# Kernel tuning notes

Measured on AMD Instinct MI355X. Metric: run time of the kernel, lower is better.

Reference implementation:

```python
import jax, jax.numpy as jnp
import numpy as np

HEADS = 4
DIM_HEAD = 64


def _rope(x, inv_freq):
    """Interleaved rotary embedding over axis -2 (time). x: (N, h, T, d)."""
    T = x.shape[-2]
    t = jnp.arange(T, dtype=x.dtype)
    f = t[:, None] * inv_freq[None, :].astype(x.dtype)   # (T, d/2)
    f = jnp.repeat(f, 2, axis=-1)                        # (T, d), interleaved pairs
    cos, sin = jnp.cos(f), jnp.sin(f)
    x1, x2 = x[..., 0::2], x[..., 1::2]
    rot = jnp.stack([-x2, x1], axis=-1).reshape(x.shape)  # rotate_half, interleaved
    return x * cos + rot * sin


def setup_inputs() -> dict:
    key = jax.random.key(0)
    k1, k2, k3, k4 = jax.random.split(key, 4)
    B, T, H, W, D = 2, 64, 32, 32, 256
    inner = HEADS * DIM_HEAD
    x = jax.random.normal(k1, (B, T, H, W, D), dtype=jnp.float32)
    w_qkv = jax.random.normal(k2, (D, 3 * inner), dtype=jnp.float32) * 0.02
    w_out = jax.random.normal(k3, (inner, D), dtype=jnp.float32) * 0.02
    b_out = jax.random.normal(k4, (D,), dtype=jnp.float32) * 0.02
    # rotary-embedding-torch default: 1 / theta^(arange(0, d, 2)/d)
    inv_freq = (1.0 / (10000.0 ** (np.arange(0, DIM_HEAD, 2) / DIM_HEAD))).astype(np.float32)
    return {"x": x, "w_qkv": w_qkv, "w_out": w_out, "b_out": b_out,
            "inv_freq": jnp.asarray(inv_freq)}


def reference(x, w_qkv, w_out, b_out, inv_freq):
    B, T, H, W, D = x.shape
    h, d = HEADS, DIM_HEAD
    qkv = x @ w_qkv                                   # (B,T,H,W,3*inner)
    q, k, v = jnp.split(qkv, 3, axis=-1)

    def to_heads(t_):
        # B T H W (h d) -> (B H W) h T d
        t_ = t_.reshape(B, T, H, W, h, d)
        return t_.transpose(0, 2, 3, 4, 1, 5).reshape(B * H * W, h, T, d)

    q, k, v = map(to_heads, (q, k, v))
    q = _rope(q, inv_freq)
    k = _rope(k, inv_freq)

    scale = 1.0 / np.sqrt(d).astype(np.float32)
    scores = jnp.einsum('nhtd,nhsd->nhts', q, k) * scale  # (BHW, h, T, T)
    causal = jnp.tril(jnp.ones((T, T), dtype=bool))
    scores = jnp.where(causal, scores, jnp.finfo(scores.dtype).min)
    attn = jax.nn.softmax(scores, axis=-1)
    o = jnp.einsum('nhts,nhsd->nhtd', attn, v)            # (BHW, h, T, d)

    # (B H W) h T d -> B T H W (h d)
    o = o.reshape(B, H, W, h, T, d).transpose(0, 4, 1, 2, 3, 5).reshape(B, T, H, W, h * d)
    return o @ w_out + b_out
```

## Files before the change

kernel.cpp:

```cpp
#include <hip/hip_runtime.h>
#include <hip/hip_bf16.h>

typedef __bf16 bf16_t;
typedef bf16_t bf16x4 __attribute__((ext_vector_type(4)));
typedef bf16_t bf16x8 __attribute__((ext_vector_type(8)));
typedef float f32x4 __attribute__((ext_vector_type(4)));
typedef unsigned int u32;

#define MFMA16(a, b, c) __builtin_amdgcn_mfma_f32_16x16x32_bf16((a), (b), (c), 0, 0, 0)

__device__ __forceinline__ int sxi(int row, int e) { return row * 256 + (e ^ ((row & 7) << 3)); }
__device__ __forceinline__ int ski(int row, int e) { return row * 64 + (e ^ ((row & 7) << 3)); }

__device__ __forceinline__ u32 pk2(float a, float b) {
  union { bf16_t h[2]; u32 u; } x;
  x.h[0] = (bf16_t)a; x.h[1] = (bf16_t)b;
  return x.u;
}

__global__ void transpose_to_bf16(const float* __restrict__ in, bf16_t* __restrict__ outp,
                                  int K, int N) {
  __shared__ float tile[32][33];
  const int k0 = blockIdx.x * 32;
  const int n0 = blockIdx.y * 32;
  const int tx = threadIdx.x;
  const int ty = threadIdx.y;
#pragma unroll
  for (int i = 0; i < 32; i += 8)
    tile[ty + i][tx] = in[(size_t)(k0 + ty + i) * N + (n0 + tx)];
  __syncthreads();
#pragma unroll
  for (int i = 0; i < 32; i += 8)
    outp[(size_t)(n0 + ty + i) * K + (k0 + tx)] = (bf16_t)tile[tx][ty + i];
}

__global__ void rope_table(const float* __restrict__ invf, float2* __restrict__ cs) {
  const int idx = blockIdx.x * 256 + threadIdx.x;
  const int t = idx >> 5;
  const int i = idx & 31;
  const float f = (float)t * invf[i];
  cs[idx] = make_float2(cosf(f), sinf(f));
}

__global__ __launch_bounds__(256) void taa_fused(
    const float* __restrict__ x, const bf16_t* __restrict__ wqkvT,
    const bf16_t* __restrict__ woutT, const float* __restrict__ bout,
    const float2* __restrict__ ropecs, float* __restrict__ out) {
  __shared__ __attribute__((aligned(16))) bf16_t sX[64 * 256];

  const int tid = threadIdx.x;
  const int w = tid >> 6;
  const int l = tid & 63;
  const int l16 = l & 15;
  const int g = l >> 4;

  const int site = blockIdx.x;
  const int b = site >> 10;
  const int sp = site & 1023;

  const size_t TS = 1024 * 256;
  const float* xp = x + (size_t)((b * 64) * 1024 + sp) * 256;
  float* op = out + (size_t)((b * 64) * 1024 + sp) * 256;

#pragma unroll
  for (int it = 0; it < 16; ++it) {
    const int idx = tid + it * 256;
    const int t = idx >> 6;
    const int c = (idx & 63) * 4;
    const float4 v = *(const float4*)(xp + (size_t)t * TS + c);
    bf16x4 o4;
    o4[0] = (bf16_t)v.x; o4[1] = (bf16_t)v.y; o4[2] = (bf16_t)v.z; o4[3] = (bf16_t)v.w;
    *(bf16x4*)&sX[sxi(t, c)] = o4;
  }
  __syncthreads();

  u32 qtb[4][4][2];
  {
    f32x4 qt[4][4] = {};
#pragma unroll
    for (int k0 = 0; k0 < 256; k0 += 32) {
      const int ko = k0 + 8 * g;
      bf16x8 aw[4], bx[4];
#pragma unroll
      for (int m = 0; m < 4; ++m)
        aw[m] = *(const bf16x8*)&wqkvT[(size_t)(w * 64 + 16 * m + l16) * 256 + ko];
#pragma unroll
      for (int n = 0; n < 4; ++n) bx[n] = *(const bf16x8*)&sX[sxi(16 * n + l16, ko)];
#pragma unroll
      for (int m = 0; m < 4; ++m)
#pragma unroll
        for (int n = 0; n < 4; ++n) qt[m][n] = MFMA16(aw[m], bx[n], qt[m][n]);
    }
    const float qs = 0.125f * 1.44269504088896f;
#pragma unroll
    for (int m = 0; m < 4; ++m)
#pragma unroll
      for (int n = 0; n < 4; ++n)
#pragma unroll
        for (int c = 0; c < 2; ++c) {
          const float v0 = qt[m][n][2 * c], v1 = qt[m][n][2 * c + 1];
          const float2 cs = ropecs[(16 * n + l16) * 32 + 8 * m + 2 * g + c];
          qtb[m][n][c] = pk2((v0 * cs.x - v1 * cs.y) * qs, (v1 * cs.x + v0 * cs.y) * qs);
        }
  }

  u32 kb[4][4][2];
  {
    f32x4 ka[4][4] = {};
#pragma unroll
    for (int k0 = 0; k0 < 256; k0 += 32) {
      const int ko = k0 + 8 * g;
      bf16x8 ax[4];
#pragma unroll
      for (int m = 0; m < 4; ++m) ax[m] = *(const bf16x8*)&sX[sxi(16 * m + l16, ko)];
#pragma unroll
      for (int n = 0; n < 4; ++n) {
        const bf16x8 bw = *(const bf16x8*)&wqkvT[(size_t)(256 + w * 64 + 16 * n + l16) * 256 + ko];
#pragma unroll
        for (int m = 0; m < 4; ++m) ka[m][n] = MFMA16(ax[m], bw, ka[m][n]);
      }
    }
#pragma unroll
    for (int m = 0; m < 4; ++m)
#pragma unroll
      for (int n = 0; n < 4; ++n) {
        f32x4 kr;
#pragma unroll
        for (int r = 0; r < 4; ++r) {
          const float v = ka[m][n][r];
          const float p = __shfl_xor(v, 1);
          const int s = 16 * m + 4 * g + r;
          const int dd = 16 * n + l16;
          const float2 cs = ropecs[s * 32 + 8 * n + (l16 >> 1)];
          kr[r] = (dd & 1) ? (v * cs.x + p * cs.y) : (v * cs.x - p * cs.y);
        }
#pragma unroll
        for (int c = 0; c < 2; ++c) kb[m][n][c] = pk2(kr[2 * c], kr[2 * c + 1]);
      }
  }

  u32 vb[4][4][2];
  {
    f32x4 va[4][4] = {};
#pragma unroll
    for (int k0 = 0; k0 < 256; k0 += 32) {
      const int ko = k0 + 8 * g;
      bf16x8 ax[4];
#pragma unroll
      for (int m = 0; m < 4; ++m) ax[m] = *(const bf16x8*)&sX[sxi(16 * m + l16, ko)];
#pragma unroll
      for (int n = 0; n < 4; ++n) {
        const bf16x8 bw = *(const bf16x8*)&wqkvT[(size_t)(512 + w * 64 + 16 * n + l16) * 256 + ko];
#pragma unroll
        for (int m = 0; m < 4; ++m) va[m][n] = MFMA16(ax[m], bw, va[m][n]);
      }
    }
#pragma unroll
    for (int m = 0; m < 4; ++m)
#pragma unroll
      for (int n = 0; n < 4; ++n)
#pragma unroll
        for (int c = 0; c < 2; ++c) vb[m][n][c] = pk2(va[m][n][2 * c], va[m][n][2 * c + 1]);
  }
  __syncthreads();

  bf16_t* slice = &sX[w * 4096];
#pragma unroll
  for (int m = 0; m < 4; ++m)
#pragma unroll
    for (int n = 0; n < 4; ++n)
#pragma unroll
      for (int c = 0; c < 2; ++c) {
        union { u32 u; bf16_t h[2]; } uz;
        uz.u = kb[m][n][c];
        slice[ski(16 * m + 4 * g + 2 * c, 16 * n + l16)] = uz.h[0];
        slice[ski(16 * m + 4 * g + 2 * c + 1, 16 * n + l16)] = uz.h[1];
      }

  f32x4 sc[4][4] = {};
#pragma unroll
  for (int ks = 0; ks < 2; ++ks) {
    const int ko = ks * 32 + 8 * g;
    bf16x8 ak[4];
#pragma unroll
    for (int m = 0; m < 4; ++m) ak[m] = *(const bf16x8*)&slice[ski(16 * m + l16, ko)];
#pragma unroll
    for (int n = 0; n < 4; ++n) {
      union { u32 u[4]; bf16x8 v; } uu;
#pragma unroll
      for (int k2 = 0; k2 < 4; ++k2) {
        const int src = ((((2 * g + (k2 >> 1)) & 3) << 4) | l16);
        const u32 a0 = (u32)__shfl((int)qtb[2 * ks][n][k2 & 1], src);
        const u32 a1 = (u32)__shfl((int)qtb[2 * ks + 1][n][k2 & 1], src);
        uu.u[k2] = (g & 2) ? a1 : a0;
      }
#pragma unroll
      for (int m = 0; m < 4; ++m) sc[m][n] = MFMA16(ak[m], uu.v, sc[m][n]);
    }
  }

#pragma unroll
  for (int n = 0; n < 4; ++n) {
    const int t = 16 * n + l16;
    float vals[16];
    float mx = -3.0e38f;
#pragma unroll
    for (int m = 0; m < 4; ++m)
#pragma unroll
      for (int r = 0; r < 4; ++r) {
        const int s = 16 * m + 4 * g + r;
        const float v = (s <= t) ? sc[m][n][r] : -3.0e38f;
        vals[4 * m + r] = v;
        mx = fmaxf(mx, v);
      }
    mx = fmaxf(mx, __shfl_xor(mx, 16));
    mx = fmaxf(mx, __shfl_xor(mx, 32));
    float sum = 0.f;
#pragma unroll
    for (int i = 0; i < 16; ++i) {
      vals[i] = exp2f(vals[i] - mx);
      sum += vals[i];
    }
    sum += __shfl_xor(sum, 16);
    sum += __shfl_xor(sum, 32);
    const float inv = 1.0f / sum;
#pragma unroll
    for (int m = 0; m < 4; ++m) {
      bf16x4 p4;
#pragma unroll
      for (int r = 0; r < 4; ++r) p4[r] = (bf16_t)(vals[4 * m + r] * inv);
      *(bf16x4*)&slice[ski(t, 16 * m + 4 * g)] = p4;
    }
  }

  f32x4 oacc[4][4] = {};
#pragma unroll
  for (int ks = 0; ks < 2; ++ks) {
    const int ko = ks * 32 + 8 * g;
    bf16x8 ap[4];
#pragma unroll
    for (int m = 0; m < 4; ++m) ap[m] = *(const bf16x8*)&slice[ski(16 * m + l16, ko)];
#pragma unroll
    for (int n = 0; n < 4; ++n) {
      union { u32 u[4]; bf16x8 v; } uu;
#pragma unroll
      for (int k2 = 0; k2 < 4; ++k2) {
        const int src = ((((2 * g + (k2 >> 1)) & 3) << 4) | l16);
        const u32 a0 = (u32)__shfl((int)vb[2 * ks][n][k2 & 1], src);
        const u32 a1 = (u32)__shfl((int)vb[2 * ks + 1][n][k2 & 1], src);
        uu.u[k2] = (g & 2) ? a1 : a0;
      }
#pragma unroll
      for (int m = 0; m < 4; ++m) oacc[m][n] = MFMA16(ap[m], uu.v, oacc[m][n]);
    }
  }
  __syncthreads();

#pragma unroll
  for (int m = 0; m < 4; ++m)
#pragma unroll
    for (int n = 0; n < 4; ++n)
#pragma unroll
      for (int r = 0; r < 4; ++r)
        sX[sxi(16 * m + 4 * g + r, w * 64 + 16 * n + l16)] = (bf16_t)oacc[m][n][r];
  __syncthreads();

  f32x4 acc[4][4] = {};
#pragma unroll
  for (int k0 = 0; k0 < 256; k0 += 32) {
    const int ko = k0 + 8 * g;
    bf16x8 af[4];
#pragma unroll
    for (int m = 0; m < 4; ++m) af[m] = *(const bf16x8*)&sX[sxi(16 * m + l16, ko)];
#pragma unroll
    for (int n = 0; n < 4; ++n) {
      const bf16x8 bw = *(const bf16x8*)&woutT[(size_t)(w * 64 + 16 * n + l16) * 256 + ko];
#pragma unroll
      for (int m = 0; m < 4; ++m) acc[m][n] = MFMA16(af[m], bw, acc[m][n]);
    }
  }
  float bb[4];
#pragma unroll
  for (int n = 0; n < 4; ++n) bb[n] = bout[w * 64 + 16 * n + l16];
#pragma unroll
  for (int m = 0; m < 4; ++m)
#pragma unroll
    for (int n = 0; n < 4; ++n)
#pragma unroll
      for (int r = 0; r < 4; ++r) {
        const int t = 16 * m + 4 * g + r;
        const int col = w * 64 + 16 * n + l16;
        op[(size_t)t * TS + col] = acc[m][n][r] + bb[n];
      }
}

extern "C" void kernel_launch(void* const* d_in, const int* in_sizes, int n_in,
                              void* d_out, int out_size, void* d_ws, size_t ws_size,
                              hipStream_t stream) {
  const float* x = (const float*)d_in[0];
  const float* wqkv = (const float*)d_in[1];
  const float* wout = (const float*)d_in[2];
  const float* bout = (const float*)d_in[3];
  const float* invf = (const float*)d_in[4];
  float* out = (float*)d_out;

  char* ws = (char*)d_ws;
  bf16_t* wqkvT = (bf16_t*)ws;
  bf16_t* woutT = (bf16_t*)(ws + 393216);
  float2* ropecs = (float2*)(ws + 393216 + 131072);

  transpose_to_bf16<<<dim3(8, 24), dim3(32, 8), 0, stream>>>(wqkv, wqkvT, 256, 768);
  transpose_to_bf16<<<dim3(8, 8), dim3(32, 8), 0, stream>>>(wout, woutT, 256, 256);
  rope_table<<<8, 256, 0, stream>>>(invf, ropecs);

  taa_fused<<<2048, 256, 0, stream>>>(x, wqkvT, woutT, bout, ropecs, out);
}
```

Baseline: 282.7 us.

## Split each head across two waves and stage K/V through shared memory

Each block now runs 512 threads, so each head is handled by two waves that each own half of the query/key time rows. This halves the per-wave accumulator register footprint. K and V are written to shared memory instead of being held in registers and exchanged by shuffles. A second 32KB LDS buffer and extra barriers are added, trading LDS use and synchronisation for lower register pressure and more resident waves per CU.

Result: slower. 336.3 us (+19.0%).

```diff
diff --git a/kernel.cpp b/kernel.cpp
--- a/kernel.cpp
+++ b/kernel.cpp
@@ -42,14 +42,17 @@
   cs[idx] = make_float2(cosf(f), sinf(f));
 }
 
-__global__ __launch_bounds__(256) void taa_fused(
+__global__ __launch_bounds__(512, 4) void taa_fused(
     const float* __restrict__ x, const bf16_t* __restrict__ wqkvT,
     const bf16_t* __restrict__ woutT, const float* __restrict__ bout,
     const float2* __restrict__ ropecs, float* __restrict__ out) {
-  __shared__ __attribute__((aligned(16))) bf16_t sX[64 * 256];
+  __shared__ __attribute__((aligned(16))) bf16_t sA[64 * 256];
+  __shared__ __attribute__((aligned(16))) bf16_t sB[64 * 256];
 
   const int tid = threadIdx.x;
-  const int w = tid >> 6;
+  const int wid = tid >> 6;
+  const int h = wid >> 1;
+  const int hf = wid & 1;
   const int l = tid & 63;
   const int l16 = l & 15;
   const int g = l >> 4;
@@ -63,129 +66,113 @@
   float* op = out + (size_t)((b * 64) * 1024 + sp) * 256;
 
 #pragma unroll
-  for (int it = 0; it < 16; ++it) {
-    const int idx = tid + it * 256;
+  for (int it = 0; it < 8; ++it) {
+    const int idx = tid + it * 512;
     const int t = idx >> 6;
     const int c = (idx & 63) * 4;
     const float4 v = *(const float4*)(xp + (size_t)t * TS + c);
     bf16x4 o4;
     o4[0] = (bf16_t)v.x; o4[1] = (bf16_t)v.y; o4[2] = (bf16_t)v.z; o4[3] = (bf16_t)v.w;
-    *(bf16x4*)&sX[sxi(t, c)] = o4;
-  }
-  __syncthreads();
-
-  u32 qtb[4][4][2];
+    *(bf16x4*)&sA[sxi(t, c)] = o4;
+  }
+  __syncthreads();
+
+  u32 qtb[4][2][2];
   {
-    f32x4 qt[4][4] = {};
+    f32x4 qt[4][2] = {};
 #pragma unroll
     for (int k0 = 0; k0 < 256; k0 += 32) {
       const int ko = k0 + 8 * g;
-      bf16x8 aw[4], bx[4];
+      bf16x8 aw[4], bx[2];
 #pragma unroll
       for (int m = 0; m < 4; ++m)
-        aw[m] = *(const bf16x8*)&wqkvT[(size_t)(w * 64 + 16 * m + l16) * 256 + ko];
-#pragma unroll
-      for (int n = 0; n < 4; ++n) bx[n] = *(const bf16x8*)&sX[sxi(16 * n + l16, ko)];
+        aw[m] = *(const bf16x8*)&wqkvT[(size_t)(h * 64 + 16 * m + l16) * 256 + ko];
+#pragma unroll
+      for (int n = 0; n < 2; ++n) bx[n] = *(const bf16x8*)&sA[sxi(hf * 32 + 16 * n + l16, ko)];
 #pragma unroll
       for (int m = 0; m < 4; ++m)
 #pragma unroll
-        for (int n = 0; n < 4; ++n) qt[m][n] = MFMA16(aw[m], bx[n], qt[m][n]);
+        for (int n = 0; n < 2; ++n) qt[m][n] = MFMA16(aw[m], bx[n], qt[m][n]);
     }
     const float qs = 0.125f * 1.44269504088896f;
 #pragma unroll
     for (int m = 0; m < 4; ++m)
 #pragma unroll
-      for (int n = 0; n < 4; ++n)
+      for (int n = 0; n < 2; ++n)
 #pragma unroll
         for (int c = 0; c < 2; ++c) {
           const float v0 = qt[m][n][2 * c], v1 = qt[m][n][2 * c + 1];
-          const float2 cs = ropecs[(16 * n + l16) * 32 + 8 * m + 2 * g + c];
+          const int tg = hf * 32 + 16 * n + l16;
+          const float2 cs = ropecs[tg * 32 + 8 * m + 2 * g + c];
           qtb[m][n][c] = pk2((v0 * cs.x - v1 * cs.y) * qs, (v1 * cs.x + v0 * cs.y) * qs);
         }
   }
 
-  u32 kb[4][4][2];
   {
-    f32x4 ka[4][4] = {};
+    f32x4 ka[2][4] = {};
 #pragma unroll
     for (int k0 = 0; k0 < 256; k0 += 32) {
       const int ko = k0 + 8 * g;
-      bf16x8 ax[4];
-#pragma unroll
-      for (int m = 0; m < 4; ++m) ax[m] = *(const bf16x8*)&sX[sxi(16 * m + l16, ko)];
+      bf16x8 ax[2];
+#pragma unroll
+      for (int m = 0; m < 2; ++m) ax[m] = *(const bf16x8*)&sA[sxi(hf * 32 + 16 * m + l16, ko)];
 #pragma unroll
       for (int n = 0; n < 4; ++n) {
-        const bf16x8 bw = *(const bf16x8*)&wqkvT[(size_t)(256 + w * 64 + 16 * n + l16) * 256 + ko];
-#pragma unroll
-        for (int m = 0; m < 4; ++m) ka[m][n] = MFMA16(ax[m], bw, ka[m][n]);
+        const bf16x8 bw = *(const bf16x8*)&wqkvT[(size_t)(256 + h * 64 + 16 * n + l16) * 256 + ko];
+#pragma unroll
+        for (int m = 0; m < 2; ++m) ka[m][n] = MFMA16(ax[m], bw, ka[m][n]);
       }
     }
 #pragma unroll
-    for (int m = 0; m < 4; ++m)
-#pragma unroll
-      for (int n = 0; n < 4; ++n) {
-        f32x4 kr;
+    for (int m = 0; m < 2; ++m)
+#pragma unroll
+      for (int n = 0; n < 4; ++n)
 #pragma unroll
         for (int r = 0; r < 4; ++r) {
           const float v = ka[m][n][r];
           const float p = __shfl_xor(v, 1);
-          const int s = 16 * m + 4 * g + r;
+          const int s = hf * 32 + 16 * m + 4 * g + r;
           const int dd = 16 * n + l16;
           const float2 cs = ropecs[s * 32 + 8 * n + (l16 >> 1)];
-          kr[r] = (dd & 1) ? (v * cs.x + p * cs.y) : (v * cs.x - p * cs.y);
+          const float o = (dd & 1) ? (v * cs.x + p * cs.y) : (v * cs.x - p * cs.y);
+          sB[h * 4096 + ski(s, dd)] = (bf16_t)o;
         }
-#pragma unroll
-        for (int c = 0; c < 2; ++c) kb[m][n][c] = pk2(kr[2 * c], kr[2 * c + 1]);
-      }
-  }
-
-  u32 vb[4][4][2];
-  {
-    f32x4 va[4][4] = {};
-#pragma unroll
-    for (int k0 = 0; k0 < 256; k0 += 32) {
-      const int ko = k0 + 8 * g;
-      bf16x8 ax[4];
-#pragma unroll
-      for (int m = 0; m < 4; ++m) ax[m] = *(const bf16x8*)&sX[sxi(16 * m + l16, ko)];
-#pragma unroll
-      for (int n = 0; n < 4; ++n) {
-        const bf16x8 bw = *(const bf16x8*)&wqkvT[(size_t)(512 + w * 64 + 16 * n + l16) * 256 + ko];
-#pragma unroll
-        for (int m = 0; m < 4; ++m) va[m][n] = MFMA16(ax[m], bw, va[m][n]);
-      }
-    }
-#pragma unroll
-    for (int m = 0; m < 4; ++m)
-#pragma unroll
-      for (int n = 0; n < 4; ++n)
-#pragma unroll
-        for (int c = 0; c < 2; ++c) vb[m][n][c] = pk2(va[m][n][2 * c], va[m][n][2 * c + 1]);
-  }
-  __syncthreads();
-
-  bf16_t* slice = &sX[w * 4096];
-#pragma unroll
-  for (int m = 0; m < 4; ++m)
+  }
+
+  f32x4 va[2][4] = {};
+#pragma unroll
+  for (int k0 = 0; k0 < 256; k0 += 32) {
+    const int ko = k0 + 8 * g;
+    bf16x8 ax[2];
+#pragma unroll
+    for (int m = 0; m < 2; ++m) ax[m] = *(const bf16x8*)&sA[sxi(hf * 32 + 16 * m + l16, ko)];
+#pragma unroll
+    for (int n = 0; n < 4; ++n) {
+      const bf16x8 bw = *(const bf16x8*)&wqkvT[(size_t)(512 + h * 64 + 16 * n + l16) * 256 + ko];
+#pragma unroll
+      for (int m = 0; m < 2; ++m) va[m][n] = MFMA16(ax[m], bw, va[m][n]);
+    }
+  }
+  __syncthreads();
+
+#pragma unroll
+  for (int m = 0; m < 2; ++m)
 #pragma unroll
     for (int n = 0; n < 4; ++n)
 #pragma unroll
-      for (int c = 0; c < 2; ++c) {
-        union { u32 u; bf16_t h[2]; } uz;
-        uz.u = kb[m][n][c];
-        slice[ski(16 * m + 4 * g + 2 * c, 16 * n + l16)] = uz.h[0];
-        slice[ski(16 * m + 4 * g + 2 * c + 1, 16 * n + l16)] = uz.h[1];
-      }
-
-  f32x4 sc[4][4] = {};
+      for (int r = 0; r < 4; ++r)
+        sA[h * 4096 + ski(16 * n + l16, hf * 32 + 16 * m + 4 * g + r)] = (bf16_t)va[m][n][r];
+  __syncthreads();
+
+  f32x4 sc[4][2] = {};
 #pragma unroll
   for (int ks = 0; ks < 2; ++ks) {
     const int ko = ks * 32 + 8 * g;
     bf16x8 ak[4];
 #pragma unroll
-    for (int m = 0; m < 4; ++m) ak[m] = *(const bf16x8*)&slice[ski(16 * m + l16, ko)];
-#pragma unroll
-    for (int n = 0; n < 4; ++n) {
+    for (int m = 0; m < 4; ++m) ak[m] = *(const bf16x8*)&sB[h * 4096 + ski(16 * m + l16, ko)];
+#pragma unroll
+    for (int n = 0; n < 2; ++n) {
       union { u32 u[4]; bf16x8 v; } uu;
 #pragma unroll
       for (int k2 = 0; k2 < 4; ++k2) {
@@ -198,10 +185,11 @@
       for (int m = 0; m < 4; ++m) sc[m][n] = MFMA16(ak[m], uu.v, sc[m][n]);
     }
   }
-
-#pragma unroll
-  for (int n = 0; n < 4; ++n) {
-    const int t = 16 * n + l16;
+  __syncthreads();
+
+#pragma unroll
+  for (int n = 0; n < 2; ++n) {
+    const int t = hf * 32 + 16 * n + l16;
     float vals[16];
     float mx = -3.0e38f;
 #pragma unroll
@@ -229,67 +217,62 @@
       bf16x4 p4;
 #pragma unroll
       for (int r = 0; r < 4; ++r) p4[r] = (bf16_t)(vals[4 * m + r] * inv);
-      *(bf16x4*)&slice[ski(t, 16 * m + 4 * g)] = p4;
-    }
-  }
-
-  f32x4 oacc[4][4] = {};
+      *(bf16x4*)&sB[h * 4096 + ski(t, 16 * m + 4 * g)] = p4;
+    }
+  }
+
+  f32x4 oacc[2][4] = {};
 #pragma unroll
   for (int ks = 0; ks < 2; ++ks) {
     const int ko = ks * 32 + 8 * g;
-    bf16x8 ap[4];
-#pragma unroll
-    for (int m = 0; m < 4; ++m) ap[m] = *(const bf16x8*)&slice[ski(16 * m + l16, ko)];
-#pragma unroll
-    for (int n = 0; n < 4; ++n) {
-      union { u32 u[4]; bf16x8 v; } uu;
-#pragma unroll
-      for (int k2 = 0; k2 < 4; ++k2) {
-        const int src = ((((2 * g + (k2 >> 1)) & 3) << 4) | l16);
-        const u32 a0 = (u32)__shfl((int)vb[2 * ks][n][k2 & 1], src);
-        const u32 a1 = (u32)__shfl((int)vb[2 * ks + 1][n][k2 & 1], src);
-        uu.u[k2] = (g & 2) ? a1 : a0;
-      }
-#pragma unroll
-      for (int m = 0; m < 4; ++m) oacc[m][n] = MFMA16(ap[m], uu.v, oacc[m][n]);
-    }
-  }
-  __syncthreads();
-
-#pragma unroll
-  for (int m = 0; m < 4; ++m)
+    bf16x8 ap[2], bv[4];
+#pragma unroll
+    for (int m = 0; m < 2; ++m)
+      ap[m] = *(const bf16x8*)&sB[h * 4096 + ski(hf * 32 + 16 * m + l16, ko)];
 #pragma unroll
     for (int n = 0; n < 4; ++n)
+      bv[n] = *(const bf16x8*)&sA[h * 4096 + ski(16 * n + l16, ko)];
+#pragma unroll
+    for (int m = 0; m < 2; ++m)
+#pragma unroll
+      for (int n = 0; n < 4; ++n) oacc[m][n] = MFMA16(ap[m], bv[n], oacc[m][n]);
+  }
+  __syncthreads();
+
+#pragma unroll
+  for (int m = 0; m < 2; ++m)
+#pragma unroll
+    for (int n = 0; n < 4; ++n)
 #pragma unroll
       for (int r = 0; r < 4; ++r)
-        sX[sxi(16 * m + 4 * g + r, w * 64 + 16 * n + l16)] = (bf16_t)oacc[m][n][r];
-  __syncthreads();
-
-  f32x4 acc[4][4] = {};
+        sB[sxi(hf * 32 + 16 * m + 4 * g + r, h * 64 + 16 * n + l16)] = (bf16_t)oacc[m][n][r];
+  __syncthreads();
+
+  f32x4 acc[4][2] = {};
 #pragma unroll
   for (int k0 = 0; k0 < 256; k0 += 32) {
     const int ko = k0 + 8 * g;
     bf16x8 af[4];
 #pragma unroll
-    for (int m = 0; m < 4; ++m) af[m] = *(const bf16x8*)&sX[sxi(16 * m + l16, ko)];
-#pragma unroll
-    for (int n = 0; n < 4; ++n) {
-      const bf16x8 bw = *(const bf16x8*)&woutT[(size_t)(w * 64 + 16 * n + l16) * 256 + ko];
+    for (int m = 0; m < 4; ++m) af[m] = *(const bf16x8*)&sB[sxi(16 * m + l16, ko)];
+#pragma unroll
+    for (int n = 0; n < 2; ++n) {
+      const bf16x8 bw = *(const bf16x8*)&woutT[(size_t)(wid * 32 + 16 * n + l16) * 256 + ko];
 #pragma unroll
       for (int m = 0; m < 4; ++m) acc[m][n] = MFMA16(af[m], bw, acc[m][n]);
     }
   }
-  float bb[4];
-#pragma unroll
-  for (int n = 0; n < 4; ++n) bb[n] = bout[w * 64 + 16 * n + l16];
+  float bb[2];
+#pragma unroll
+  for (int n = 0; n < 2; ++n) bb[n] = bout[wid * 32 + 16 * n + l16];
 #pragma unroll
   for (int m = 0; m < 4; ++m)
 #pragma unroll
-    for (int n = 0; n < 4; ++n)
+    for (int n = 0; n < 2; ++n)
 #pragma unroll
       for (int r = 0; r < 4; ++r) {
         const int t = 16 * m + 4 * g + r;
-        const int col = w * 64 + 16 * n + l16;
+        const int col = wid * 32 + 16 * n + l16;
         op[(size_t)t * TS + col] = acc[m][n][r] + bb[n];
       }
 }
@@ -313,5 +296,5 @@
   transpose_to_bf16<<<dim3(8, 8), dim3(32, 8), 0, stream>>>(wout, woutT, 256, 256);
   rope_table<<<8, 256, 0, stream>>>(invf, ropecs);
 
-  taa_fused<<<2048, 256, 0, stream>>>(x, wqkvT, woutT, bout, ropecs, out);
-}
+  taa_fused<<<2048, 512, 0, stream>>>(x, wqkvT, woutT, bout, ropecs, out);
+}
```
